# Optimization experiments

Measured on AMD Instinct MI355X. Metric: run time of the kernel, lower is better.

The kernel has to match this reference:

```python
import jax, jax.numpy as jnp
import numpy as np

T, B, V, E, H = 256, 64, 10000, 400, 1152


def _n(k, shape, scale=0.05):
    return jax.random.normal(k, shape, jnp.float32) * scale


def setup_inputs() -> dict:
    key = jax.random.key(0)
    ks = jax.random.split(key, 32)
    inp = {}
    inp["x"] = jax.random.randint(ks[0], (T, B), 0, V)
    inp["h0"] = _n(ks[1], (B, H)); inp["h1"] = _n(ks[2], (B, H)); inp["h2"] = _n(ks[3], (B, E))
    inp["c0"] = _n(ks[4], (B, H)); inp["c1"] = _n(ks[5], (B, H)); inp["c2"] = _n(ks[6], (B, E))
    inp["emb"] = _n(ks[7], (V, E), 0.1)
    # layer i: (input_dim, output_dim): (E,H), (H,H), (H,E)
    sizes = [(E, H), (H, H), (H, E)]
    j = 8
    for i, (din, dout) in enumerate(sizes):
        inp[f"W_ih{i}"] = _n(ks[j], (4 * dout, din)); j += 1
        inp[f"W_hh{i}"] = _n(ks[j], (4 * dout, dout)); j += 1
        inp[f"b_ih{i}"] = _n(ks[j], (4 * dout,)); j += 1
        inp[f"b_hh{i}"] = _n(ks[j], (4 * dout,)); j += 1
    inp["dec_W"] = _n(ks[j], (V, E)); j += 1
    inp["dec_b"] = jnp.zeros((V,), jnp.float32)
    return inp


def lstm_cell(x, h, c, Wih, Whh, bih, bhh):
    # PyTorch LSTMCell: gates = x@Wih^T + bih + h@Whh^T + bhh, order i,f,g,o
    g = x @ Wih.T + h @ Whh.T + bih + bhh
    i, f, gg, o = jnp.split(g, 4, axis=-1)
    c2 = jax.nn.sigmoid(f) * c + jax.nn.sigmoid(i) * jnp.tanh(gg)
    h2 = jax.nn.sigmoid(o) * jnp.tanh(c2)
    return h2, c2


def reference(x, h0, h1, h2, c0, c1, c2, emb,
              W_ih0, W_hh0, b_ih0, b_hh0,
              W_ih1, W_hh1, b_ih1, b_hh1,
              W_ih2, W_hh2, b_ih2, b_hh2,
              dec_W, dec_b):
    xe = emb[x]  # [T, B, E]

    def step(carry, xt):
        a0, a1, a2, s0, s1, s2 = carry
        a0, s0 = lstm_cell(xt, a0, s0, W_ih0, W_hh0, b_ih0, b_hh0)
        a1, s1 = lstm_cell(a0, a1, s1, W_ih1, W_hh1, b_ih1, b_hh1)
        a2, s2 = lstm_cell(a1, a2, s2, W_ih2, W_hh2, b_ih2, b_hh2)
        return (a0, a1, a2, s0, s1, s2), a2

    _, out = jax.lax.scan(step, (h0, h1, h2, c0, c1, c2), xe)  # out: [T, B, E]
    decoded = out @ dec_W.T + dec_b  # [T, B, V]
    return decoded
```

## Files before the change

### kernel.cpp

```cpp
#include <hip/hip_runtime.h>
#include <hip/hip_bf16.h>

typedef __hip_bfloat16 bf16;
typedef __attribute__((ext_vector_type(8))) short short8;
typedef __attribute__((ext_vector_type(4))) float f32x4;

#define T_ 256
#define B_ 64
#define V_ 10000
#define E_ 400
#define H_ 1152
#define KU 2304
#define XW 416
#define KD 416
#define XET (XW*B_)
#define NBLK 169

#define MFMA16 __builtin_amdgcn_mfma_f32_16x16x32_bf16
#define ATL(p) __hip_atomic_load((p), __ATOMIC_RELAXED, __HIP_MEMORY_SCOPE_AGENT)
#define ATS(p, v) __hip_atomic_store((p), (v), __ATOMIC_RELAXED, __HIP_MEMORY_SCOPE_AGENT)
#define PIN(x) asm volatile("" : "+v"(x))


__global__ __launch_bounds__(256) void prep_wint(
    const float* __restrict__ s1, int w1,
    const float* __restrict__ s2, int off2, int w2, int Hl,
    bf16* __restrict__ dst, long total)
{
    long i = (long)blockIdx.x * 256 + threadIdx.x;
    if (i >= total) return;
    int r = (int)(i / KU), k = (int)(i % KU);
    int hcol = r >> 2, gate = r & 3;
    long srow = (long)gate * Hl + hcol;
    float v = 0.f;
    if (k < w1) v = s1[srow * w1 + k];
    else if (k >= off2 && k < off2 + w2) v = s2[srow * w2 + (k - off2)];
    dst[i] = __float2bfloat16(v);
}

__global__ __launch_bounds__(256) void prep_wcat(
    const float* __restrict__ s1, int w1,
    bf16* __restrict__ dst, int Ktot, long total)
{
    long i = (long)blockIdx.x * 256 + threadIdx.x;
    if (i >= total) return;
    int k = (int)(i % Ktot);
    long n = i / Ktot;
    dst[i] = __float2bfloat16(k < w1 ? s1[n * w1 + k] : 0.f);
}

__global__ __launch_bounds__(256) void bias_int(
    const float* __restrict__ a, const float* __restrict__ b,
    int Hl, float* __restrict__ d, int n)
{
    int r = blockIdx.x * 256 + threadIdx.x;
    if (r >= n) return;
    int hcol = r >> 2, gate = r & 3;
    d[r] = a[gate * Hl + hcol] + b[gate * Hl + hcol];
}

__global__ __launch_bounds__(256) void gather_xef(
    const int* __restrict__ x, const float* __restrict__ emb,
    bf16* __restrict__ XEf)
{
    long i = (long)blockIdx.x * 256 + threadIdx.x;
    if (i >= (long)T_ * B_ * XW) return;
    int k = (int)(i % XW);
    int b = (int)((i / XW) % B_);
    int t = (int)(i / ((long)XW * B_));
    float v = (k < E_) ? emb[(long)x[t * B_ + b] * E_ + k] : 0.f;
    XEf[(long)t * XET + (((k >> 3) * 64 + b) << 3) + (k & 7)] = __float2bfloat16(v);
}

__global__ __launch_bounds__(256) void copy_hf(
    const float* __restrict__ src, bf16* __restrict__ dst, int cols, int total)
{
    int i = blockIdx.x * 256 + threadIdx.x;
    if (i >= total) return;
    int k = i % cols, b = i / cols;
    dst[(((k >> 3) * 64 + b) << 3) + (k & 7)] = __float2bfloat16(src[(long)b * cols + k]);
}

__global__ __launch_bounds__(256) void copy_f32(
    const float* __restrict__ src, float* __restrict__ dst, int n)
{
    int i = blockIdx.x * 256 + threadIdx.x;
    if (i < n) dst[i] = src[i];
}

__device__ __forceinline__ void grid_bar(int* flags, int* gen, int phase) {
    asm volatile("s_waitcnt vmcnt(0)" ::: "memory");
    __syncthreads();
    if (blockIdx.x == 0) {
        if (threadIdx.x < 64) {
            const int ln = threadIdx.x;
            if (ln == 0) ATS(&flags[0], phase);
            for (;;) {
                int f0 = (ln       < NBLK) ? ATL(&flags[ln])       : phase;
                int f1 = (ln + 64  < NBLK) ? ATL(&flags[ln + 64])  : phase;
                int f2 = (ln + 128 < NBLK) ? ATL(&flags[ln + 128]) : phase;
                if (__all(f0 >= phase && f1 >= phase && f2 >= phase)) break;
                __builtin_amdgcn_s_sleep(1);
            }
            if (ln == 0) {
                ATS(gen, phase);
                __builtin_amdgcn_fence(__ATOMIC_ACQUIRE, "agent");
            }
        }
    } else {
        if (threadIdx.x == 0) {
            ATS(&flags[blockIdx.x], phase);
            while (ATL(gen) < phase)
                __builtin_amdgcn_s_sleep(1);
            __builtin_amdgcn_fence(__ATOMIC_ACQUIRE, "agent");
        }
    }
    __syncthreads();
    asm volatile("" ::: "memory");
}

struct Frag4 { short8 f0, f1, f2, f3; };

__global__ __launch_bounds__(512, 2) void awd_persistent(
    const bf16* __restrict__ XEf,
    const bf16* __restrict__ W0, const bf16* __restrict__ W1, const bf16* __restrict__ W2,
    const float* __restrict__ b0, const float* __restrict__ b1, const float* __restrict__ b2,
    bf16* H0f0, bf16* H0f1, bf16* H1f0, bf16* H1f1, bf16* H2f0, bf16* H2f1,
    float* c0, float* c1, float* c2, bf16* OUTB,
    int* flags, int* gen)
{
    __shared__ float gsm[2][4][64][65];
    __shared__ unsigned short hsm[64][24];
    const int bid = blockIdx.x;
    const int tid = threadIdx.x;
    const int lane = tid & 63;
    const int w8 = tid >> 6;
    const int lh = lane >> 4, l15 = lane & 15;
    const int boff8 = (lh * 64 + l15) * 8;

    int layer, grp;
    if (bid < 72)       { layer = 1; grp = bid; }
    else if (bid < 144) { layer = 0; grp = bid - 72; }
    else                { layer = 2; grp = bid - 144; }

    const bf16* Wp  = (layer == 0) ? W0 : (layer == 1) ? W1 : W2;
    const float* bias = (layer == 0) ? b0 : (layer == 1) ? b1 : b2;
    const float* cbuf = (layer == 0) ? c0 : (layer == 1) ? c1 : c2;
    const int Hl  = (layer == 2) ? 400 : 1152;
    const int bkt = (layer == 0) ? 13 : 36;
    const int nkt = (layer == 1) ? 72 : 49;
    const int KT  = (layer == 1) ? 9  : 7;
    const int kbase = w8 * KT;

    short8 wreg[9][4];
    #pragma unroll
    for (int u = 0; u < 9; ++u)
        if (u < KT) {
            #pragma unroll
            for (int rt = 0; rt < 4; ++rt) {
                int row = grp * 64 + rt * 16 + l15;
                int k   = (kbase + u) * 32 + lh * 8;
                wreg[u][rt] = *(const short8*)(Wp + (long)row * KU + k);
                PIN(wreg[u][rt]);
            }
        }

    float myb[2][4];
    #pragma unroll
    for (int e = 0; e < 2; ++e)
        #pragma unroll
        for (int g = 0; g < 4; ++g)
            myb[e][g] = bias[grp * 64 + (w8 + e * 8) * 4 + g];

    float creg[2];
    #pragma unroll
    for (int e = 0; e < 2; ++e)
        creg[e] = cbuf[(long)lane * Hl + grp * 16 + w8 + e * 8];

    for (int s = -1; s <= 256; ++s) {
        bool active = (layer == 0) ? (s <= 254)
                    : (layer == 1) ? (s >= 0 && s <= 255)
                                   : (s >= 1);
        if (active) {
            const int p = s & 1, q = p ^ 1;
            const bf16 *A1, *A2; bf16* hfW; bf16* ob = nullptr;
            if (layer == 0) {
                A1 = XEf + (long)(s + 1) * XET;
                A2 = p ? H0f1 : H0f0;
                hfW = q ? H0f1 : H0f0;
            } else if (layer == 1) {
                A1 = p ? H0f1 : H0f0;
                A2 = q ? H1f1 : H1f0;
                hfW = p ? H1f1 : H1f0;
            } else {
                A1 = q ? H1f1 : H1f0;
                A2 = p ? H2f1 : H2f0;
                hfW = q ? H2f1 : H2f0;
                ob = OUTB + (long)(s - 1) * B_ * XW;
            }

            auto loadf = [&](int u) -> Frag4 {
                const int ktg = kbase + u;
                const bf16* src; int ktL;
                if (ktg < bkt)      { src = A1; ktL = ktg; }
                else if (ktg < nkt) { src = A2; ktL = ktg - bkt; }
                else                { src = A1; ktL = 0; }
                const bf16* pB = src + ktL * 2048 + boff8;
                Frag4 r;
                r.f0 = *(const short8*)(pB);
                r.f1 = *(const short8*)(pB + 128);
                r.f2 = *(const short8*)(pB + 256);
                r.f3 = *(const short8*)(pB + 384);
                return r;
            };

            f32x4 acc[4][4];
            #pragma unroll
            for (int rt = 0; rt < 4; ++rt)
                #pragma unroll
                for (int m = 0; m < 4; ++m)
                    acc[rt][m] = (f32x4){0.f, 0.f, 0.f, 0.f};

            auto domfma = [&](int u, const Frag4& f) {
                #pragma unroll
                for (int rt = 0; rt < 4; ++rt) {
                    acc[rt][0] = MFMA16(wreg[u][rt], f.f0, acc[rt][0], 0, 0, 0);
                    acc[rt][1] = MFMA16(wreg[u][rt], f.f1, acc[rt][1], 0, 0, 0);
                    acc[rt][2] = MFMA16(wreg[u][rt], f.f2, acc[rt][2], 0, 0, 0);
                    acc[rt][3] = MFMA16(wreg[u][rt], f.f3, acc[rt][3], 0, 0, 0);
                }
            };

            #pragma unroll
            for (int u = 0; u < 9; ++u)
                if (u < KT) {
                    Frag4 f = loadf(u);
                    domfma(u, f);
                }

            #pragma unroll
            for (int rt = 0; rt < 4; ++rt)
                #pragma unroll
                for (int m = 0; m < 4; ++m)
                    #pragma unroll
                    for (int r = 0; r < 4; ++r)
                        gsm[w8 >> 2][w8 & 3][rt * 16 + lh * 4 + r][m * 16 + l15] = acc[rt][m][r];
            __syncthreads();

            #pragma unroll
            for (int e = 0; e < 2; ++e) {
                int b = lane;
                int cl = w8 + e * 8;
                float gv[4];
                #pragma unroll
                for (int g = 0; g < 4; ++g) {
                    float v = myb[e][g];
                    #pragma unroll
                    for (int kq = 0; kq < 4; ++kq)
                        v += gsm[0][kq][cl * 4 + g][b] + gsm[1][kq][cl * 4 + g][b];
                    gv[g] = v;
                }
                float c_old = creg[e];
                float i_s = 1.f / (1.f + expf(-gv[0]));
                float f_s = 1.f / (1.f + expf(-gv[1]));
                float o_s = 1.f / (1.f + expf(-gv[3]));
                float c_new = f_s * c_old + i_s * tanhf(gv[2]);
                float hval = o_s * tanhf(c_new);
                creg[e] = c_new;
                bf16 hb = __float2bfloat16(hval);
                unsigned short hbits;
                __builtin_memcpy(&hbits, &hb, 2);
                hsm[b][cl] = hbits;
            }
            __syncthreads();

            if (w8 < 2) {
                unsigned long long v0, v1;
                __builtin_memcpy(&v0, &hsm[lane][w8 * 8], 8);
                __builtin_memcpy(&v1, &hsm[lane][w8 * 8 + 4], 8);
                unsigned long long* qp =
                    (unsigned long long*)(hfW + (((long)grp * 2 + w8) * 64 + lane) * 8);
                ATS(qp, v0);
                ATS(qp + 1, v1);
            } else if (w8 == 2 && layer == 2) {
                short8 v0 = *(const short8*)&hsm[lane][0];
                short8 v1 = *(const short8*)&hsm[lane][8];
                *(short8*)(ob + (long)lane * XW + grp * 16) = v0;
                *(short8*)(ob + (long)lane * XW + grp * 16 + 8) = v1;
            }
        }
        grid_bar(flags, gen, s + 2);
    }
}

__global__ __launch_bounds__(256) void decoder(
    const bf16* __restrict__ A, const bf16* __restrict__ W,
    const float* __restrict__ bias, float* __restrict__ out)
{
    const int tid = threadIdx.x;
    const int lane = tid & 63;
    const int w = tid >> 6;
    const int mw = w >> 1, nw = w & 1;
    const int n0 = blockIdx.x * 128 + nw * 64;
    const int m0 = blockIdx.y * 128 + mw * 64;
    const int c16 = lane & 15;
    const int kg = lane >> 4;

    f32x4 acc[4][4];
    #pragma unroll
    for (int mi = 0; mi < 4; ++mi)
        #pragma unroll
        for (int ns = 0; ns < 4; ++ns)
            acc[mi][ns] = (f32x4){0.f, 0.f, 0.f, 0.f};

    int nrow[4];
    #pragma unroll
    for (int ns = 0; ns < 4; ++ns) {
        int n = n0 + ns * 16 + c16;
        nrow[ns] = (n < V_) ? n : (V_ - 1);
    }

    const bf16* arow = A + (long)(m0 + c16) * KD + kg * 8;
    #pragma unroll
    for (int kt = 0; kt < 13; ++kt) {
        short8 af[4], bf[4];
        #pragma unroll
        for (int mi = 0; mi < 4; ++mi)
            af[mi] = *(const short8*)(arow + (long)mi * 16 * KD + kt * 32);
        #pragma unroll
        for (int ns = 0; ns < 4; ++ns)
            bf[ns] = *(const short8*)(W + (long)nrow[ns] * KD + kt * 32 + kg * 8);
        #pragma unroll
        for (int mi = 0; mi < 4; ++mi)
            #pragma unroll
            for (int ns = 0; ns < 4; ++ns)
                acc[mi][ns] = MFMA16(af[mi], bf[ns], acc[mi][ns], 0, 0, 0);
    }

    #pragma unroll
    for (int mi = 0; mi < 4; ++mi)
        #pragma unroll
        for (int ns = 0; ns < 4; ++ns) {
            int col = n0 + ns * 16 + c16;
            if (col < V_) {
                float bv = bias[col];
                #pragma unroll
                for (int r = 0; r < 4; ++r) {
                    int row = m0 + mi * 16 + kg * 4 + r;
                    out[(size_t)row * V_ + col] = acc[mi][ns][r] + bv;
                }
            }
        }
}


extern "C" void kernel_launch(void* const* d_in, const int* in_sizes, int n_in,
                              void* d_out, int out_size, void* d_ws, size_t ws_size,
                              hipStream_t stream)
{
    const int*   x    = (const int*)d_in[0];
    const float* h0   = (const float*)d_in[1];
    const float* h1   = (const float*)d_in[2];
    const float* h2   = (const float*)d_in[3];
    const float* c0   = (const float*)d_in[4];
    const float* c1   = (const float*)d_in[5];
    const float* c2   = (const float*)d_in[6];
    const float* emb  = (const float*)d_in[7];
    const float* Wih0 = (const float*)d_in[8];
    const float* Whh0 = (const float*)d_in[9];
    const float* bih0 = (const float*)d_in[10];
    const float* bhh0 = (const float*)d_in[11];
    const float* Wih1 = (const float*)d_in[12];
    const float* Whh1 = (const float*)d_in[13];
    const float* bih1 = (const float*)d_in[14];
    const float* bhh1 = (const float*)d_in[15];
    const float* Wih2 = (const float*)d_in[16];
    const float* Whh2 = (const float*)d_in[17];
    const float* bih2 = (const float*)d_in[18];
    const float* bhh2 = (const float*)d_in[19];
    const float* decW = (const float*)d_in[20];
    const float* decb = (const float*)d_in[21];

    char* wsb = (char*)d_ws;
    size_t off = 0;
    auto alloc = [&](size_t bytes) -> void* {
        void* ptr = wsb + off;
        off = (off + bytes + 255) & ~(size_t)255;
        return ptr;
    };

    bf16* W0i = (bf16*)alloc((size_t)4608 * KU * 2);
    bf16* W1i = (bf16*)alloc((size_t)4608 * KU * 2);
    bf16* W2i = (bf16*)alloc((size_t)1600 * KU * 2);
    bf16* Wdc = (bf16*)alloc((size_t)V_ * KD * 2);
    float* b0i = (float*)alloc(4608 * 4);
    float* b1i = (float*)alloc(4608 * 4);
    float* b2i = (float*)alloc(1600 * 4);
    bf16* XEf = (bf16*)alloc((size_t)T_ * XET * 2);
    bf16* H0f0 = (bf16*)alloc((size_t)B_ * H_ * 2);
    bf16* H0f1 = (bf16*)alloc((size_t)B_ * H_ * 2);
    bf16* H1f0 = (bf16*)alloc((size_t)B_ * H_ * 2);
    bf16* H1f1 = (bf16*)alloc((size_t)B_ * H_ * 2);
    bf16* H2f0 = (bf16*)alloc((size_t)B_ * XW * 2);
    bf16* H2f1 = (bf16*)alloc((size_t)B_ * XW * 2);
    float* c0b = (float*)alloc((size_t)B_ * H_ * 4);
    float* c1b = (float*)alloc((size_t)B_ * H_ * 4);
    float* c2b = (float*)alloc((size_t)B_ * E_ * 4);
    bf16* OUTB = (bf16*)alloc((size_t)T_ * B_ * XW * 2);
    int* gbar = (int*)alloc(2048);

    auto cdiv = [](long a, long b) { return (int)((a + b - 1) / b); };

    hipMemsetAsync(gbar, 0, 2048, stream);

    prep_wint<<<cdiv(4608L * KU, 256), 256, 0, stream>>>(Wih0, 400,  Whh0, 416,  1152, 1152, W0i, 4608L * KU);
    prep_wint<<<cdiv(4608L * KU, 256), 256, 0, stream>>>(Wih1, 1152, Whh1, 1152, 1152, 1152, W1i, 4608L * KU);
    prep_wint<<<cdiv(1600L * KU, 256), 256, 0, stream>>>(Wih2, 1152, Whh2, 1152, 400,  400,  W2i, 1600L * KU);
    prep_wcat<<<cdiv((long)V_ * KD, 256), 256, 0, stream>>>(decW, 400, Wdc, KD, (long)V_ * KD);
    bias_int<<<cdiv(4608, 256), 256, 0, stream>>>(bih0, bhh0, 1152, b0i, 4608);
    bias_int<<<cdiv(4608, 256), 256, 0, stream>>>(bih1, bhh1, 1152, b1i, 4608);
    bias_int<<<cdiv(1600, 256), 256, 0, stream>>>(bih2, bhh2, 400,  b2i, 1600);
    gather_xef<<<cdiv((long)T_ * B_ * XW, 256), 256, 0, stream>>>(x, emb, XEf);

    hipMemsetAsync(H2f0, 0, (size_t)B_ * XW * 2, stream);
    hipMemsetAsync(H2f1, 0, (size_t)B_ * XW * 2, stream);
    hipMemsetAsync(OUTB, 0, (size_t)T_ * B_ * XW * 2, stream);

    copy_hf<<<cdiv(B_ * H_, 256), 256, 0, stream>>>(h0, H0f1, H_, B_ * H_);
    copy_hf<<<cdiv(B_ * H_, 256), 256, 0, stream>>>(h1, H1f1, H_, B_ * H_);
    copy_hf<<<cdiv(B_ * E_, 256), 256, 0, stream>>>(h2, H2f1, E_, B_ * E_);
    copy_f32<<<cdiv(B_ * H_, 256), 256, 0, stream>>>(c0, c0b, B_ * H_);
    copy_f32<<<cdiv(B_ * H_, 256), 256, 0, stream>>>(c1, c1b, B_ * H_);
    copy_f32<<<cdiv(B_ * E_, 256), 256, 0, stream>>>(c2, c2b, B_ * E_);

    {
        int* flags = gbar;
        int* gen   = gbar + 448;
        void* args[] = {
            (void*)&XEf, (void*)&W0i, (void*)&W1i, (void*)&W2i,
            (void*)&b0i, (void*)&b1i, (void*)&b2i,
            (void*)&H0f0, (void*)&H0f1, (void*)&H1f0, (void*)&H1f1,
            (void*)&H2f0, (void*)&H2f1,
            (void*)&c0b, (void*)&c1b, (void*)&c2b, (void*)&OUTB,
            (void*)&flags, (void*)&gen
        };
        hipLaunchCooperativeKernel((void*)awd_persistent, dim3(NBLK), dim3(512),
                                   args, 0, stream);
    }

    decoder<<<dim3((V_ + 127) / 128, (T_ * B_) / 128), 256, 0, stream>>>(
        OUTB, Wdc, decb, (float*)d_out);
}
```

Before: 3.157 ms.

## Stage activations via global_load_lds, halve reduction smem, vectorize weight prep

Weight-prep kernels now convert eight floats per thread and write them as 16-byte stores, where before each thread wrote a single element. In the persistent LSTM kernel, activation fragments are staged into LDS with global_load_lds in pairs, then read back from LDS for the MFMAs. Every warp now processes a fixed 9 k-tiles, with extra tiles pointing at zero-padded weights. The cross-warp gate reduction now uses a two-phase accumulate into a single gsm buffer, which halves its shared memory but adds a barrier. Waiting on vmcnt(0) after each pair serializes loads with compute, and layers 0 and 2 do wasted MFMA work on the padding.

```diff
diff --git a/kernel.cpp b/kernel.cpp
--- a/kernel.cpp
+++ b/kernel.cpp
@@ -22,31 +22,49 @@
 #define PIN(x) asm volatile("" : "+v"(x))
 
 
-__global__ __launch_bounds__(256) void prep_wint(
+__global__ __launch_bounds__(256) void prep_wint8(
     const float* __restrict__ s1, int w1,
     const float* __restrict__ s2, int off2, int w2, int Hl,
-    bf16* __restrict__ dst, long total)
+    bf16* __restrict__ dst, long total8)
 {
     long i = (long)blockIdx.x * 256 + threadIdx.x;
-    if (i >= total) return;
-    int r = (int)(i / KU), k = (int)(i % KU);
-    int hcol = r >> 2, gate = r & 3;
+    if (i >= total8) return;
+    const int KB = KU / 8;
+    int kb = (int)(i % KB) * 8;
+    long r = i / KB;
+    int hcol = (int)(r >> 2), gate = (int)(r & 3);
     long srow = (long)gate * Hl + hcol;
-    float v = 0.f;
-    if (k < w1) v = s1[srow * w1 + k];
-    else if (k >= off2 && k < off2 + w2) v = s2[srow * w2 + (k - off2)];
-    dst[i] = __float2bfloat16(v);
-}
-
-__global__ __launch_bounds__(256) void prep_wcat(
+    const float* src = nullptr;
+    if (kb < w1) src = s1 + srow * w1 + kb;
+    else if (kb >= off2 && kb < off2 + w2) src = s2 + srow * w2 + (kb - off2);
+    short8 v;
+    #pragma unroll
+    for (int j = 0; j < 8; ++j) {
+        bf16 b = __float2bfloat16(src ? src[j] : 0.f);
+        unsigned short us; __builtin_memcpy(&us, &b, 2);
+        v[j] = (short)us;
+    }
+    *(short8*)(dst + r * KU + kb) = v;
+}
+
+__global__ __launch_bounds__(256) void prep_wcat8(
     const float* __restrict__ s1, int w1,
-    bf16* __restrict__ dst, int Ktot, long total)
+    bf16* __restrict__ dst, int Ktot, long total8)
 {
     long i = (long)blockIdx.x * 256 + threadIdx.x;
-    if (i >= total) return;
-    int k = (int)(i % Ktot);
-    long n = i / Ktot;
-    dst[i] = __float2bfloat16(k < w1 ? s1[n * w1 + k] : 0.f);
+    if (i >= total8) return;
+    int KB = Ktot / 8;
+    int kb = (int)(i % KB) * 8;
+    long n = i / KB;
+    const float* src = (kb < w1) ? s1 + n * w1 + kb : nullptr;
+    short8 v;
+    #pragma unroll
+    for (int j = 0; j < 8; ++j) {
+        bf16 b = __float2bfloat16(src ? src[j] : 0.f);
+        unsigned short us; __builtin_memcpy(&us, &b, 2);
+        v[j] = (short)us;
+    }
+    *(short8*)(dst + n * Ktot + kb) = v;
 }
 
 __global__ __launch_bounds__(256) void bias_int(
@@ -119,8 +137,6 @@
     asm volatile("" ::: "memory");
 }
 
-struct Frag4 { short8 f0, f1, f2, f3; };
-
 __global__ __launch_bounds__(512, 2) void awd_persistent(
     const bf16* __restrict__ XEf,
     const bf16* __restrict__ W0, const bf16* __restrict__ W1, const bf16* __restrict__ W2,
@@ -129,8 +145,9 @@
     float* c0, float* c1, float* c2, bf16* OUTB,
     int* flags, int* gen)
 {
-    __shared__ float gsm[2][4][64][65];
+    __shared__ float gsm[4][64][65];
     __shared__ unsigned short hsm[64][24];
+    __shared__ char Ast[8][2][4096];
     const int bid = blockIdx.x;
     const int tid = threadIdx.x;
     const int lane = tid & 63;
@@ -149,20 +166,17 @@
     const int Hl  = (layer == 2) ? 400 : 1152;
     const int bkt = (layer == 0) ? 13 : 36;
     const int nkt = (layer == 1) ? 72 : 49;
-    const int KT  = (layer == 1) ? 9  : 7;
-    const int kbase = w8 * KT;
+    const int kbase = w8 * 9;
 
     short8 wreg[9][4];
     #pragma unroll
     for (int u = 0; u < 9; ++u)
-        if (u < KT) {
-            #pragma unroll
-            for (int rt = 0; rt < 4; ++rt) {
-                int row = grp * 64 + rt * 16 + l15;
-                int k   = (kbase + u) * 32 + lh * 8;
-                wreg[u][rt] = *(const short8*)(Wp + (long)row * KU + k);
-                PIN(wreg[u][rt]);
-            }
+        #pragma unroll
+        for (int rt = 0; rt < 4; ++rt) {
+            int row = grp * 64 + rt * 16 + l15;
+            int k   = (kbase + u) * 32 + lh * 8;
+            wreg[u][rt] = *(const short8*)(Wp + (long)row * KU + k);
+            PIN(wreg[u][rt]);
         }
 
     float myb[2][4];
@@ -199,19 +213,21 @@
                 ob = OUTB + (long)(s - 1) * B_ * XW;
             }
 
-            auto loadf = [&](int u) -> Frag4 {
+            auto stageu = [&](int u, int slot) {
                 const int ktg = kbase + u;
                 const bf16* src; int ktL;
                 if (ktg < bkt)      { src = A1; ktL = ktg; }
                 else if (ktg < nkt) { src = A2; ktL = ktg - bkt; }
                 else                { src = A1; ktL = 0; }
                 const bf16* pB = src + ktL * 2048 + boff8;
-                Frag4 r;
-                r.f0 = *(const short8*)(pB);
-                r.f1 = *(const short8*)(pB + 128);
-                r.f2 = *(const short8*)(pB + 256);
-                r.f3 = *(const short8*)(pB + 384);
-                return r;
+                char* dst = &Ast[w8][slot][0];
+                __builtin_amdgcn_global_load_lds((const void*)pB,         dst,        16, 0, 0);
+                __builtin_amdgcn_global_load_lds((const void*)(pB + 128), dst + 1024, 16, 0, 0);
+                __builtin_amdgcn_global_load_lds((const void*)(pB + 256), dst + 2048, 16, 0, 0);
+                __builtin_amdgcn_global_load_lds((const void*)(pB + 384), dst + 3072, 16, 0, 0);
+            };
+            auto rdfrag = [&](int slot, int f) -> short8 {
+                return *(const short8*)(&Ast[w8][slot][f * 1024 + lane * 16]);
             };
 
             f32x4 acc[4][4];
@@ -221,30 +237,54 @@
                 for (int m = 0; m < 4; ++m)
                     acc[rt][m] = (f32x4){0.f, 0.f, 0.f, 0.f};
 
-            auto domfma = [&](int u, const Frag4& f) {
+            auto domfma = [&](int u, short8 f0, short8 f1, short8 f2, short8 f3) {
                 #pragma unroll
                 for (int rt = 0; rt < 4; ++rt) {
-                    acc[rt][0] = MFMA16(wreg[u][rt], f.f0, acc[rt][0], 0, 0, 0);
-                    acc[rt][1] = MFMA16(wreg[u][rt], f.f1, acc[rt][1], 0, 0, 0);
-                    acc[rt][2] = MFMA16(wreg[u][rt], f.f2, acc[rt][2], 0, 0, 0);
-                    acc[rt][3] = MFMA16(wreg[u][rt], f.f3, acc[rt][3], 0, 0, 0);
+                    acc[rt][0] = MFMA16(wreg[u][rt], f0, acc[rt][0], 0, 0, 0);
+                    acc[rt][1] = MFMA16(wreg[u][rt], f1, acc[rt][1], 0, 0, 0);
+                    acc[rt][2] = MFMA16(wreg[u][rt], f2, acc[rt][2], 0, 0, 0);
+                    acc[rt][3] = MFMA16(wreg[u][rt], f3, acc[rt][3], 0, 0, 0);
                 }
             };
 
             #pragma unroll
-            for (int u = 0; u < 9; ++u)
-                if (u < KT) {
-                    Frag4 f = loadf(u);
-                    domfma(u, f);
+            for (int pr = 0; pr < 5; ++pr) {
+                const int u0 = 2 * pr, u1 = 2 * pr + 1;
+                stageu(u0, 0);
+                if (u1 < 9) stageu(u1, 1);
+                asm volatile("s_waitcnt vmcnt(0)" ::: "memory");
+                {
+                    short8 f0 = rdfrag(0, 0), f1 = rdfrag(0, 1);
+                    short8 f2 = rdfrag(0, 2), f3 = rdfrag(0, 3);
+                    domfma(u0, f0, f1, f2, f3);
                 }
-
-            #pragma unroll
-            for (int rt = 0; rt < 4; ++rt)
-                #pragma unroll
-                for (int m = 0; m < 4; ++m)
+                if (u1 < 9) {
+                    short8 f0 = rdfrag(1, 0), f1 = rdfrag(1, 1);
+                    short8 f2 = rdfrag(1, 2), f3 = rdfrag(1, 3);
+                    domfma(u1, f0, f1, f2, f3);
+                }
+            }
+
+            __syncthreads();
+            if (w8 >= 4) {
+                #pragma unroll
+                for (int rt = 0; rt < 4; ++rt)
                     #pragma unroll
-                    for (int r = 0; r < 4; ++r)
-                        gsm[w8 >> 2][w8 & 3][rt * 16 + lh * 4 + r][m * 16 + l15] = acc[rt][m][r];
+                    for (int m = 0; m < 4; ++m)
+                        #pragma unroll
+                        for (int r = 0; r < 4; ++r)
+                            gsm[w8 - 4][rt * 16 + lh * 4 + r][m * 16 + l15] = acc[rt][m][r];
+            }
+            __syncthreads();
+            if (w8 < 4) {
+                #pragma unroll
+                for (int rt = 0; rt < 4; ++rt)
+                    #pragma unroll
+                    for (int m = 0; m < 4; ++m)
+                        #pragma unroll
+                        for (int r = 0; r < 4; ++r)
+                            gsm[w8][rt * 16 + lh * 4 + r][m * 16 + l15] += acc[rt][m][r];
+            }
             __syncthreads();
 
             #pragma unroll
@@ -257,7 +297,7 @@
                     float v = myb[e][g];
                     #pragma unroll
                     for (int kq = 0; kq < 4; ++kq)
-                        v += gsm[0][kq][cl * 4 + g][b] + gsm[1][kq][cl * 4 + g][b];
+                        v += gsm[kq][cl * 4 + g][b];
                     gv[g] = v;
                 }
                 float c_old = creg[e];
@@ -413,10 +453,10 @@
 
     hipMemsetAsync(gbar, 0, 2048, stream);
 
-    prep_wint<<<cdiv(4608L * KU, 256), 256, 0, stream>>>(Wih0, 400,  Whh0, 416,  1152, 1152, W0i, 4608L * KU);
-    prep_wint<<<cdiv(4608L * KU, 256), 256, 0, stream>>>(Wih1, 1152, Whh1, 1152, 1152, 1152, W1i, 4608L * KU);
-    prep_wint<<<cdiv(1600L * KU, 256), 256, 0, stream>>>(Wih2, 1152, Whh2, 1152, 400,  400,  W2i, 1600L * KU);
-    prep_wcat<<<cdiv((long)V_ * KD, 256), 256, 0, stream>>>(decW, 400, Wdc, KD, (long)V_ * KD);
+    prep_wint8<<<cdiv(4608L * (KU/8), 256), 256, 0, stream>>>(Wih0, 400,  Whh0, 416,  1152, 1152, W0i, 4608L * (KU/8));
+    prep_wint8<<<cdiv(4608L * (KU/8), 256), 256, 0, stream>>>(Wih1, 1152, Whh1, 1152, 1152, 1152, W1i, 4608L * (KU/8));
+    prep_wint8<<<cdiv(1600L * (KU/8), 256), 256, 0, stream>>>(Wih2, 1152, Whh2, 1152, 400,  400,  W2i, 1600L * (KU/8));
+    prep_wcat8<<<cdiv((long)V_ * (KD/8), 256), 256, 0, stream>>>(decW, 400, Wdc, KD, (long)V_ * (KD/8));
     bias_int<<<cdiv(4608, 256), 256, 0, stream>>>(bih0, bhh0, 1152, b0i, 4608);
     bias_int<<<cdiv(4608, 256), 256, 0, stream>>>(bih1, bhh1, 1152, b1i, 4608);
     bias_int<<<cdiv(1600, 256), 256, 0, stream>>>(bih2, bhh2, 400,  b2i, 1600);
```

Result: slower. 3.541 ms (+12.2%).
